# Kernel tuning notes

Measured on AMD Instinct MI355X. Metric: run time of the kernel, lower is better.

The kernel has to match this reference:

```python
import jax, jax.numpy as jnp
import numpy as np

B, T, C = 16, 1024, 768
H = 12
D = C // H  # 64 head dim


def setup_inputs() -> dict:
    key = jax.random.key(0)
    k1, k2, k3, k4, k5 = jax.random.split(key, 5)
    s = 0.02
    return {
        "x": jax.random.normal(k1, (B, T, C), dtype=jnp.float32),
        "w_attn": jax.random.normal(k2, (C, 3 * C), dtype=jnp.float32) * s,
        "b_attn": jax.random.normal(k3, (3 * C,), dtype=jnp.float32) * s,
        "w_proj": jax.random.normal(k4, (C, C), dtype=jnp.float32) * s,
        "b_proj": jax.random.normal(k5, (C,), dtype=jnp.float32) * s,
    }


def reference(x, w_attn, b_attn, w_proj, b_proj):
    Bc, Tc, Cc = x.shape
    qkv = x @ w_attn + b_attn  # [B,T,3C]
    q, k, v = jnp.split(qkv, 3, axis=-1)
    # [B,T,C] -> [B,H,T,D]
    q = q.reshape(Bc, Tc, H, D).transpose(0, 2, 1, 3)
    k = k.reshape(Bc, Tc, H, D).transpose(0, 2, 1, 3)
    v = v.reshape(Bc, Tc, H, D).transpose(0, 2, 1, 3)
    scale = 1.0 / np.sqrt(D).astype(np.float32)
    atn = jnp.einsum("bhqd,bhkd->bhqk", q, k) * scale
    causal = jnp.tril(jnp.ones((Tc, Tc), dtype=bool))
    atn = jnp.where(causal[None, None], atn, -jnp.inf)
    atn = jax.nn.softmax(atn, axis=-1)
    y = jnp.einsum("bhqk,bhkd->bhqd", atn, v)
    y = y.transpose(0, 2, 1, 3).reshape(Bc, Tc, Cc)
    return y @ w_proj + b_proj
```

## Files before the change

### kernel.cpp

```cpp
#include <hip/hip_runtime.h>
#include <hip/hip_bf16.h>

typedef __attribute__((ext_vector_type(4))) float f32x4;
typedef __attribute__((ext_vector_type(8))) short s16x8;
typedef __attribute__((ext_vector_type(4))) short s16x4;

#define AS1 __attribute__((address_space(1)))
#define AS3 __attribute__((address_space(3)))

__device__ __forceinline__ short f2bf(float f) {
    union { float f; unsigned u; } a; a.f = f;
    unsigned r = a.u + 0x7fff + ((a.u >> 16) & 1);
    return (short)(r >> 16);
}

__device__ __forceinline__ unsigned pk_bf16(float a, float b) {
    unsigned r;
    asm("v_cvt_pk_bf16_f32 %0, %1, %2" : "=v"(r) : "v"(a), "v"(b));
    return r;
}


__global__ __launch_bounds__(256) void convert_f32_bf16(const float* __restrict__ in,
                                                        short* __restrict__ out, int n4) {
    int i = blockIdx.x * 256 + threadIdx.x;
    if (i < n4) {
        f32x4 v = *(const f32x4*)(in + (long)i * 4);
        s16x4 o;
        o.x = f2bf(v.x); o.y = f2bf(v.y); o.z = f2bf(v.z); o.w = f2bf(v.w);
        *(s16x4*)(out + (long)i * 4) = o;
    }
}

__global__ __launch_bounds__(256) void transpose_w(const float* __restrict__ src,
                                                   short* __restrict__ dst, int K, int N) {
    __shared__ short t[64][65];
    int k0 = blockIdx.x * 64, n0 = blockIdx.y * 64;
    int tid = threadIdx.x;
    for (int i = tid; i < 64 * 64; i += 256) {
        int r = i >> 6, c = i & 63;
        t[r][c] = f2bf(src[(long)(k0 + r) * N + n0 + c]);
    }
    __syncthreads();
    for (int i = tid; i < 64 * 64; i += 256) {
        int r = i >> 6, c = i & 63;
        dst[(long)(n0 + r) * K + k0 + c] = t[c][r];
    }
}

__global__ __launch_bounds__(256) void transpose_vp(const short* __restrict__ vp,
                                                    short* __restrict__ vt) {
    __shared__ short t[64][72];
    int t0 = blockIdx.x * 64;
    int g = blockIdx.y;
    int tid = threadIdx.x;
#pragma unroll
    for (int i = 0; i < 2; ++i) {
        int j = tid + i * 256;
        int r = j >> 3, c = j & 7;
        s16x8 v = *(const s16x8*)(vp + ((long)g * 1024 + t0 + r) * 64 + c * 8);
#pragma unroll
        for (int e = 0; e < 8; ++e) t[c * 8 + e][r] = v[e];
    }
    __syncthreads();
#pragma unroll
    for (int i = 0; i < 2; ++i) {
        int j = tid + i * 256;
        int r = j >> 3, c = j & 7;
        *(s16x8*)(vt + ((long)g * 64 + r) * 1024 + t0 + c * 8) = *(const s16x8*)&t[r][c * 8];
    }
}


template <int MODE>
__global__ __launch_bounds__(256) void gemm_bt(const short* __restrict__ A,
                                               const short* __restrict__ BT,
                                               const float* __restrict__ bias,
                                               float* __restrict__ outF,
                                               short* __restrict__ q_,
                                               short* __restrict__ k_,
                                               short* __restrict__ v_,
                                               int M, int N, int K) {
    __shared__ short lA[128 * 32];
    __shared__ short lB[128 * 32];
    int tid = threadIdx.x;
    int lane = tid & 63, w = tid >> 6;
    int wr = w >> 1, wc = w & 1;
    int lo = lane & 15, hi = lane >> 4;
    int m0 = blockIdx.y * 128, n0 = blockIdx.x * 128;

    f32x4 acc[4][4];
#pragma unroll
    for (int i = 0; i < 4; ++i)
#pragma unroll
        for (int j = 0; j < 4; ++j) acc[i][j] = (f32x4){0.f, 0.f, 0.f, 0.f};

    const short* Abase = A + (long)m0 * K;
    const short* Bbase = BT + (long)n0 * K;

    for (int k0 = 0; k0 < K; k0 += 32) {
        __syncthreads();
#pragma unroll
        for (int i = 0; i < 2; ++i) {
            int c = (w * 2 + i) * 64 + lane;
            const short* ga = Abase + (long)(c >> 2) * K + k0 + (c & 3) * 8;
            const short* gb = Bbase + (long)(c >> 2) * K + k0 + (c & 3) * 8;
            __builtin_amdgcn_global_load_lds((const AS1 void*)ga,
                                             (AS3 void*)(lA + (w * 2 + i) * 512), 16, 0, 0);
            __builtin_amdgcn_global_load_lds((const AS1 void*)gb,
                                             (AS3 void*)(lB + (w * 2 + i) * 512), 16, 0, 0);
        }
        __syncthreads();

        s16x8 a[4], b[4];
#pragma unroll
        for (int mi = 0; mi < 4; ++mi)
            a[mi] = *(const s16x8*)(lA + (wr * 64 + mi * 16 + lo) * 32 + hi * 8);
#pragma unroll
        for (int ni = 0; ni < 4; ++ni)
            b[ni] = *(const s16x8*)(lB + (wc * 64 + ni * 16 + lo) * 32 + hi * 8);
#pragma unroll
        for (int mi = 0; mi < 4; ++mi)
#pragma unroll
            for (int ni = 0; ni < 4; ++ni)
                acc[mi][ni] = __builtin_amdgcn_mfma_f32_16x16x32_bf16(a[mi], b[ni], acc[mi][ni], 0, 0, 0);
    }

#pragma unroll
    for (int mi = 0; mi < 4; ++mi)
#pragma unroll
        for (int ni = 0; ni < 4; ++ni)
#pragma unroll
            for (int r = 0; r < 4; ++r) {
                int gm = m0 + wr * 64 + mi * 16 + hi * 4 + r;
                int gn = n0 + wc * 64 + ni * 16 + lo;
                float v = acc[mi][ni][r] + bias[gn];
                if (MODE == 1) {
                    int part = gn / 768;
                    int hh = (gn - part * 768) >> 6;
                    int dd = gn & 63;
                    long gi = (((long)(gm >> 10) * 12 + hh) * 1024 + (gm & 1023)) * 64 + dd;
                    if (part == 0) q_[gi] = f2bf(v * 0.180336880f);
                    else if (part == 1) k_[gi] = f2bf(v);
                    else v_[gi] = f2bf(v);
                } else {
                    outF[(long)gm * N + gn] = v;
                }
            }
}


__device__ __forceinline__ void attn_tile(const short* __restrict__ Kb,
                                          const short* __restrict__ Vb,
                                          int kv0, int qb0, bool diag,
                                          s16x8 bq0, s16x8 bq1,
                                          f32x4 (&ov)[4], float& mrun, float& lrun,
                                          int lo, int hi, int hi2, int sA, int sB,
                                          int sl0, int sl1) {
    f32x4 s[4];
#pragma unroll
    for (int n = 0; n < 4; ++n) {
        const short* kr = Kb + (n * 16 + lo) * 64;
        s16x8 kf0 = *(const s16x8*)(kr + sl0);
        s16x8 kf1 = *(const s16x8*)(kr + sl1);
        f32x4 t = (f32x4){0.f, 0.f, 0.f, 0.f};
        t = __builtin_amdgcn_mfma_f32_16x16x32_bf16(kf0, bq0, t, 0, 0, 0);
        t = __builtin_amdgcn_mfma_f32_16x16x32_bf16(kf1, bq1, t, 0, 0, 0);
        s[n] = t;
    }
    s16x8 av0[4], av1[4];
#pragma unroll
    for (int nd = 0; nd < 4; ++nd) {
        const short* vr = Vb + (nd * 16 + lo) * 64;
        av0[nd] = *(const s16x8*)(vr + sl0);
        av1[nd] = *(const s16x8*)(vr + sl1);
    }

    int qglob = qb0 + lo;
    if (diag) {
#pragma unroll
        for (int n = 0; n < 4; ++n)
#pragma unroll
            for (int r = 0; r < 4; ++r)
                if (kv0 + n * 16 + hi * 4 + r > qglob) s[n][r] = -3.0e38f;
    }
    float mx = s[0][0];
#pragma unroll
    for (int n = 0; n < 4; ++n)
#pragma unroll
        for (int r = 0; r < 4; ++r) mx = fmaxf(mx, s[n][r]);
    mx = fmaxf(mx, __shfl_xor(mx, 16));
    mx = fmaxf(mx, __shfl_xor(mx, 32));
    float mn = fmaxf(mrun, mx);
    float alpha = exp2f(mrun - mn);
    mrun = mn;
    float rs = 0.f;
#pragma unroll
    for (int n = 0; n < 4; ++n)
#pragma unroll
        for (int r = 0; r < 4; ++r) {
            float p = exp2f(s[n][r] - mn);
            s[n][r] = p;
            rs += p;
        }
    rs += __shfl_xor(rs, 16);
    rs += __shfl_xor(rs, 32);
    lrun = lrun * alpha + rs;
#pragma unroll
    for (int nd = 0; nd < 4; ++nd)
#pragma unroll
        for (int r = 0; r < 4; ++r) ov[nd][r] *= alpha;

    unsigned W[4][2];
#pragma unroll
    for (int n = 0; n < 4; ++n) {
        W[n][0] = pk_bf16(s[n][0], s[n][1]);
        W[n][1] = pk_bf16(s[n][2], s[n][3]);
    }
    s16x8 ap[2];
#pragma unroll
    for (int kc = 0; kc < 2; ++kc) {
        unsigned a0 = __shfl(W[kc * 2][0], sA), b0 = __shfl(W[kc * 2 + 1][0], sA);
        unsigned a1 = __shfl(W[kc * 2][1], sA), b1 = __shfl(W[kc * 2 + 1][1], sA);
        unsigned a2 = __shfl(W[kc * 2][0], sB), b2 = __shfl(W[kc * 2 + 1][0], sB);
        unsigned a3 = __shfl(W[kc * 2][1], sB), b3 = __shfl(W[kc * 2 + 1][1], sB);
        union { unsigned u[4]; s16x8 v; } cv;
        cv.u[0] = hi2 ? b0 : a0;
        cv.u[1] = hi2 ? b1 : a1;
        cv.u[2] = hi2 ? b2 : a2;
        cv.u[3] = hi2 ? b3 : a3;
        ap[kc] = cv.v;
    }
#pragma unroll
    for (int nd = 0; nd < 4; ++nd) {
        ov[nd] = __builtin_amdgcn_mfma_f32_16x16x32_bf16(av0[nd], ap[0], ov[nd], 0, 0, 0);
        ov[nd] = __builtin_amdgcn_mfma_f32_16x16x32_bf16(av1[nd], ap[1], ov[nd], 0, 0, 0);
    }
}

__device__ __forceinline__ void store_out(const f32x4 (&ov)[4], float lrun,
                                          long rowbase, int qb0, int h,
                                          int lo, int hi, short* __restrict__ y) {
    float inv = 1.0f / lrun;
    long row = (rowbase + qb0 + lo) * 768 + h * 64;
#pragma unroll
    for (int nd = 0; nd < 4; ++nd)
#pragma unroll
        for (int j2 = 0; j2 < 2; ++j2) {
            unsigned pv = pk_bf16(ov[nd][2 * j2] * inv, ov[nd][2 * j2 + 1] * inv);
            *(unsigned*)(y + row + nd * 16 + hi * 4 + 2 * j2) = pv;
        }
}

__global__ __launch_bounds__(256) void flash_attn7(const short* __restrict__ qpk,
                                                   const short* __restrict__ kpk,
                                                   const short* __restrict__ vtg,
                                                   short* __restrict__ y) {
    __shared__ short Kb[2][4096];
    __shared__ short Vb[2][4096];

    int d = blockIdx.x;
    int qp = d / 192, g = d % 192;
    int h = g % 12, b = g / 12;
    int tid = threadIdx.x, lane = tid & 63, w = tid >> 6;
    int lo = lane & 15, hi = lane >> 4, hi2 = hi >> 1;
    long rowbase = (long)b * 1024;
    const short* kb_g = kpk + (long)g * 65536;
    const short* vt_g = vtg + (long)g * 65536;
    int sA = ((hi & 1) * 2) * 16 + lo, sB = sA + 16;

    int rl = lane >> 3;
    int cs8 = (((lane & 7) ^ rl)) * 8;
    int r0 = w * 8 + rl;
    int sl0 = (hi ^ (lo & 7)) * 8;
    int sl1 = ((hi + 4) ^ (lo & 7)) * 8;

    int qbA = qp * 64 + w * 16;
    int qbB = (15 - qp) * 64 + w * 16;

    f32x4 ov[4];
    float mrun = -3.0e38f, lrun = 0.f;
#pragma unroll
    for (int nd = 0; nd < 4; ++nd) ov[nd] = (f32x4){0.f, 0.f, 0.f, 0.f};
    s16x8 bq0, bq1;
    {
        const short* qrow = qpk + ((long)g * 1024 + qbA + lo) * 64;
        bq0 = *(const s16x8*)(qrow + hi * 8);
        bq1 = *(const s16x8*)(qrow + 32 + hi * 8);
    }

#define STAGE(kv0_, buf_)                                                                    \
    do {                                                                                     \
        _Pragma("unroll")                                                                    \
        for (int i_ = 0; i_ < 2; ++i_) {                                                     \
            int r_ = i_ * 32 + r0;                                                           \
            __builtin_amdgcn_global_load_lds(                                                \
                (const AS1 void*)(kb_g + (long)((kv0_) + r_) * 64 + cs8),                    \
                (AS3 void*)(Kb[buf_] + (i_ * 32 + w * 8) * 64), 16, 0, 0);                   \
            __builtin_amdgcn_global_load_lds(                                                \
                (const AS1 void*)(vt_g + (long)r_ * 1024 + (kv0_) + cs8),                    \
                (AS3 void*)(Vb[buf_] + (i_ * 32 + w * 8) * 64), 16, 0, 0);                   \
        }                                                                                    \
    } while (0)

    STAGE(0, 0);
    __syncthreads();

    int cur = 0;
    for (int u = 0; u < 17; ++u) {
        int nu = u + 1;
        if (nu < 17) {
            int nkv0 = (nu <= qp) ? nu * 64 : (nu - qp - 1) * 64;
            STAGE(nkv0, cur ^ 1);
        }
        bool phaseA = (u <= qp);
        int kv0 = phaseA ? u * 64 : (u - qp - 1) * 64;
        int qb0 = phaseA ? qbA : qbB;
        bool diag = phaseA ? (u == qp) : (u == 16);
        attn_tile(Kb[cur], Vb[cur], kv0, qb0, diag, bq0, bq1, ov, mrun, lrun,
                  lo, hi, hi2, sA, sB, sl0, sl1);
        if (phaseA && u == qp) {
            store_out(ov, lrun, rowbase, qbA, h, lo, hi, y);
            const short* qrow = qpk + ((long)g * 1024 + qbB + lo) * 64;
            bq0 = *(const s16x8*)(qrow + hi * 8);
            bq1 = *(const s16x8*)(qrow + 32 + hi * 8);
#pragma unroll
            for (int nd = 0; nd < 4; ++nd) ov[nd] = (f32x4){0.f, 0.f, 0.f, 0.f};
            mrun = -3.0e38f; lrun = 0.f;
        }
        __syncthreads();
        cur ^= 1;
    }
    store_out(ov, lrun, rowbase, qbB, h, lo, hi, y);
#undef STAGE
}


extern "C" void kernel_launch(void* const* d_in, const int* in_sizes, int n_in,
                              void* d_out, int out_size, void* d_ws, size_t ws_size,
                              hipStream_t stream) {
    const float* x      = (const float*)d_in[0];
    const float* w_attn = (const float*)d_in[1];
    const float* b_attn = (const float*)d_in[2];
    const float* w_proj = (const float*)d_in[3];
    const float* b_proj = (const float*)d_in[4];

    char* ws = (char*)d_ws;
    short* x_bf = (short*)ws;
    short* qpk  = (short*)(ws + 25165824);
    short* kpk  = (short*)(ws + 50331648);
    short* vpk  = (short*)(ws + 75497472);
    short* yb   = (short*)(ws + 100663296);
    short* waT  = (short*)(ws + 125829120);
    short* wpT  = (short*)(ws + 129368064);
    short* vt   = x_bf;

    convert_f32_bf16<<<dim3(12288), dim3(256), 0, stream>>>(x, x_bf, 3145728);
    transpose_w<<<dim3(12, 36), dim3(256), 0, stream>>>(w_attn, waT, 768, 2304);
    transpose_w<<<dim3(12, 12), dim3(256), 0, stream>>>(w_proj, wpT, 768, 768);
    gemm_bt<1><<<dim3(18, 128), dim3(256), 0, stream>>>(x_bf, waT, b_attn,
                                                        (float*)nullptr, qpk, kpk, vpk,
                                                        16384, 2304, 768);
    transpose_vp<<<dim3(16, 192), dim3(256), 0, stream>>>(vpk, vt);
    flash_attn7<<<dim3(1536), dim3(256), 0, stream>>>(qpk, kpk, vt, yb);
    gemm_bt<0><<<dim3(6, 128), dim3(256), 0, stream>>>(yb, wpT, b_proj,
                                                       (float*)d_out, (short*)nullptr,
                                                       (short*)nullptr, (short*)nullptr,
                                                       16384, 768, 768);
}
```

Before: 238.1 us.

## Rewrite GEMM as 256x256 tile, 8-wave double-buffered pipelined kernel with swizzled LDS

Replaces the 128x128, 4-wave GEMM, which synchronised twice per K step, with a 256x256 tile computed by 512 threads. Global-to-LDS loads are double-buffered and issued ahead of use, with vmcnt waits and raw barriers instead of __syncthreads. The LDS layout is XOR-swizzled to avoid bank conflicts, and s_setprio is raised around the MFMA blocks. This targets load latency and barrier stalls in the QKV and projection GEMMs. The cost is far fewer blocks (576 and 192), which risks poor occupancy across the CUs, especially for the projection GEMM.

```diff
diff --git a/kernel.cpp b/kernel.cpp
--- a/kernel.cpp
+++ b/kernel.cpp
@@ -73,67 +73,108 @@
 
 
 template <int MODE>
-__global__ __launch_bounds__(256) void gemm_bt(const short* __restrict__ A,
-                                               const short* __restrict__ BT,
-                                               const float* __restrict__ bias,
-                                               float* __restrict__ outF,
-                                               short* __restrict__ q_,
-                                               short* __restrict__ k_,
-                                               short* __restrict__ v_,
-                                               int M, int N, int K) {
-    __shared__ short lA[128 * 32];
-    __shared__ short lB[128 * 32];
+__global__ __launch_bounds__(512, 2) void gemm_bt(const short* __restrict__ A,
+                                                  const short* __restrict__ BT,
+                                                  const float* __restrict__ bias,
+                                                  float* __restrict__ outF,
+                                                  short* __restrict__ q_,
+                                                  short* __restrict__ k_,
+                                                  short* __restrict__ v_,
+                                                  int M, int N, int K) {
+    __shared__ short As[2 * 2 * 64 * 64];
+    __shared__ short Bs[2 * 2 * 64 * 64];
+
     int tid = threadIdx.x;
     int lane = tid & 63, w = tid >> 6;
-    int wr = w >> 1, wc = w & 1;
+    int wm = w >> 2, wn = w & 3;
     int lo = lane & 15, hi = lane >> 4;
-    int m0 = blockIdx.y * 128, n0 = blockIdx.x * 128;
-
-    f32x4 acc[4][4];
-#pragma unroll
-    for (int i = 0; i < 4; ++i)
+    int m0 = blockIdx.y * 256, n0 = blockIdx.x * 256;
+    int T = K >> 5;
+
+    int srlo = lo >> 1;
+    int aoff = srlo * 64 + ((((lo & 1) << 2) + hi) ^ srlo) * 8;
+
+    int srl = w * 8 + (lane >> 3);
+    int cc = (lane & 7) ^ (lane >> 3);
+    int growoff = cc >> 2;
+    int gcoloff = (cc & 3) * 8;
+
+    const short* Ag = A + (long)m0 * K;
+    const short* Bg = BT + (long)n0 * K;
+
+    f32x4 acc[8][4];
+#pragma unroll
+    for (int i = 0; i < 8; ++i)
 #pragma unroll
         for (int j = 0; j < 4; ++j) acc[i][j] = (f32x4){0.f, 0.f, 0.f, 0.f};
 
-    const short* Abase = A + (long)m0 * K;
-    const short* Bbase = BT + (long)n0 * K;
-
-    for (int k0 = 0; k0 < K; k0 += 32) {
-        __syncthreads();
-#pragma unroll
-        for (int i = 0; i < 2; ++i) {
-            int c = (w * 2 + i) * 64 + lane;
-            const short* ga = Abase + (long)(c >> 2) * K + k0 + (c & 3) * 8;
-            const short* gb = Bbase + (long)(c >> 2) * K + k0 + (c & 3) * 8;
-            __builtin_amdgcn_global_load_lds((const AS1 void*)ga,
-                                             (AS3 void*)(lA + (w * 2 + i) * 512), 16, 0, 0);
-            __builtin_amdgcn_global_load_lds((const AS1 void*)gb,
-                                             (AS3 void*)(lB + (w * 2 + i) * 512), 16, 0, 0);
+    auto stage = [&](int tt, const short* G, short* Ls, int eta) {
+        const short* src = G + (long)(eta * 128 + srl * 2 + growoff) * K + tt * 32 + gcoloff;
+        short* dst = Ls + (((tt & 1) * 2 + eta) * 64 + w * 8) * 64;
+        __builtin_amdgcn_global_load_lds((const AS1 void*)src, (AS3 void*)dst, 16, 0, 0);
+    };
+
+    stage(0, Ag, As, 0); stage(0, Ag, As, 1);
+    stage(0, Bg, Bs, 0); stage(0, Bg, Bs, 1);
+    stage(1, Bg, Bs, 0); stage(1, Bg, Bs, 1);
+    stage(1, Ag, As, 0);
+    asm volatile("s_waitcnt vmcnt(3)" ::: "memory");
+    __builtin_amdgcn_s_barrier();
+
+    for (int t = 0; t < T; ++t) {
+        int buf = t & 1;
+        s16x8 bfr[4], afr[4];
+#pragma unroll
+        for (int ni = 0; ni < 4; ++ni)
+            bfr[ni] = *(const s16x8*)(Bs + ((buf * 2 + (wn >> 1)) * 64 + (wn & 1) * 32 + ni * 8) * 64 + aoff);
+#pragma unroll
+        for (int mi = 0; mi < 4; ++mi)
+            afr[mi] = *(const s16x8*)(As + ((buf * 2 + 0) * 64 + wm * 32 + mi * 8) * 64 + aoff);
+        if (t + 1 < T) stage(t + 1, Ag, As, 1);
+        __builtin_amdgcn_s_barrier();
+        asm volatile("s_waitcnt lgkmcnt(0)" ::: "memory");
+        __builtin_amdgcn_sched_barrier(0);
+        __builtin_amdgcn_s_setprio(1);
+#pragma unroll
+        for (int mi = 0; mi < 4; ++mi)
+#pragma unroll
+            for (int ni = 0; ni < 4; ++ni)
+                acc[mi][ni] = __builtin_amdgcn_mfma_f32_16x16x32_bf16(afr[mi], bfr[ni], acc[mi][ni], 0, 0, 0);
+        __builtin_amdgcn_s_setprio(0);
+        __builtin_amdgcn_s_barrier();
+
+#pragma unroll
+        for (int mi = 0; mi < 4; ++mi)
+            afr[mi] = *(const s16x8*)(As + ((buf * 2 + 1) * 64 + wm * 32 + mi * 8) * 64 + aoff);
+        if (t + 2 < T) {
+            stage(t + 2, Bg, Bs, 0);
+            stage(t + 2, Bg, Bs, 1);
+            stage(t + 2, Ag, As, 0);
+            asm volatile("s_waitcnt vmcnt(3)" ::: "memory");
+        } else if (t + 1 < T) {
+            asm volatile("s_waitcnt vmcnt(0)" ::: "memory");
         }
-        __syncthreads();
-
-        s16x8 a[4], b[4];
+        __builtin_amdgcn_s_barrier();
+        asm volatile("s_waitcnt lgkmcnt(0)" ::: "memory");
+        __builtin_amdgcn_sched_barrier(0);
+        __builtin_amdgcn_s_setprio(1);
 #pragma unroll
         for (int mi = 0; mi < 4; ++mi)
-            a[mi] = *(const s16x8*)(lA + (wr * 64 + mi * 16 + lo) * 32 + hi * 8);
+#pragma unroll
+            for (int ni = 0; ni < 4; ++ni)
+                acc[mi + 4][ni] = __builtin_amdgcn_mfma_f32_16x16x32_bf16(afr[mi], bfr[ni], acc[mi + 4][ni], 0, 0, 0);
+        __builtin_amdgcn_s_setprio(0);
+        __builtin_amdgcn_s_barrier();
+    }
+
+#pragma unroll
+    for (int mi = 0; mi < 8; ++mi)
 #pragma unroll
         for (int ni = 0; ni < 4; ++ni)
-            b[ni] = *(const s16x8*)(lB + (wc * 64 + ni * 16 + lo) * 32 + hi * 8);
-#pragma unroll
-        for (int mi = 0; mi < 4; ++mi)
-#pragma unroll
-            for (int ni = 0; ni < 4; ++ni)
-                acc[mi][ni] = __builtin_amdgcn_mfma_f32_16x16x32_bf16(a[mi], b[ni], acc[mi][ni], 0, 0, 0);
-    }
-
-#pragma unroll
-    for (int mi = 0; mi < 4; ++mi)
-#pragma unroll
-        for (int ni = 0; ni < 4; ++ni)
 #pragma unroll
             for (int r = 0; r < 4; ++r) {
-                int gm = m0 + wr * 64 + mi * 16 + hi * 4 + r;
-                int gn = n0 + wc * 64 + ni * 16 + lo;
+                int gm = m0 + (mi >> 2) * 128 + wm * 64 + (mi & 3) * 16 + hi * 4 + r;
+                int gn = n0 + wn * 64 + ni * 16 + lo;
                 float v = acc[mi][ni][r] + bias[gn];
                 if (MODE == 1) {
                     int part = gn / 768;
@@ -358,13 +399,13 @@
     convert_f32_bf16<<<dim3(12288), dim3(256), 0, stream>>>(x, x_bf, 3145728);
     transpose_w<<<dim3(12, 36), dim3(256), 0, stream>>>(w_attn, waT, 768, 2304);
     transpose_w<<<dim3(12, 12), dim3(256), 0, stream>>>(w_proj, wpT, 768, 768);
-    gemm_bt<1><<<dim3(18, 128), dim3(256), 0, stream>>>(x_bf, waT, b_attn,
-                                                        (float*)nullptr, qpk, kpk, vpk,
-                                                        16384, 2304, 768);
+    gemm_bt<1><<<dim3(9, 64), dim3(512), 0, stream>>>(x_bf, waT, b_attn,
+                                                      (float*)nullptr, qpk, kpk, vpk,
+                                                      16384, 2304, 768);
     transpose_vp<<<dim3(16, 192), dim3(256), 0, stream>>>(vpk, vt);
     flash_attn7<<<dim3(1536), dim3(256), 0, stream>>>(qpk, kpk, vt, yb);
-    gemm_bt<0><<<dim3(6, 128), dim3(256), 0, stream>>>(yb, wpT, b_proj,
-                                                       (float*)d_out, (short*)nullptr,
-                                                       (short*)nullptr, (short*)nullptr,
-                                                       16384, 768, 768);
-}
+    gemm_bt<0><<<dim3(3, 64), dim3(512), 0, stream>>>(yb, wpT, b_proj,
+                                                      (float*)d_out, (short*)nullptr,
+                                                      (short*)nullptr, (short*)nullptr,
+                                                      16384, 768, 768);
+}
```

Result: slower. 251.4 us (+5.6%).

## Restructure GEMM with K=64 steps, XOR-swizzled LDS, XCD block swizzle, hoisted epilogue

Applied to the files above, without the earlier changes.

The GEMM kernel now stages 64 elements of K per iteration as two 32-wide sub-tiles, halving the number of barrier pairs. The LDS layout packs two logical rows per 64-element row and XORs the column chunk to avoid bank conflicts on fragment reads. Blocks use a 1D grid remapped so consecutive blocks land on the same XCD (bid&7 interleave), which should improve L2 reuse. The epilogue hoists bias loads and the per-element q/k/v partition math out of the inner loop. The cost is more complex indexing, and the swizzle assumes the grid size is divisible by 8.

```diff
diff --git a/kernel.cpp b/kernel.cpp
--- a/kernel.cpp
+++ b/kernel.cpp
@@ -81,13 +81,18 @@
                                                short* __restrict__ k_,
                                                short* __restrict__ v_,
                                                int M, int N, int K) {
-    __shared__ short lA[128 * 32];
-    __shared__ short lB[128 * 32];
+    __shared__ short lA[2 * 64 * 64];
+    __shared__ short lB[2 * 64 * 64];
     int tid = threadIdx.x;
     int lane = tid & 63, w = tid >> 6;
     int wr = w >> 1, wc = w & 1;
     int lo = lane & 15, hi = lane >> 4;
-    int m0 = blockIdx.y * 128, n0 = blockIdx.x * 128;
+
+    int bid = blockIdx.x;
+    int swz = (bid & 7) * ((int)gridDim.x >> 3) + (bid >> 3);
+    int NX = N >> 7;
+    int bx = swz % NX, by = swz / NX;
+    int m0 = by * 128, n0 = bx * 128;
 
     f32x4 acc[4][4];
 #pragma unroll
@@ -98,55 +103,85 @@
     const short* Abase = A + (long)m0 * K;
     const short* Bbase = BT + (long)n0 * K;
 
-    for (int k0 = 0; k0 < K; k0 += 32) {
+    int lr = lane >> 3;
+    int cc = (lane & 7) ^ lr;
+    int growoff = cc >> 2;
+    int gcol = (cc & 3) * 8;
+
+    int srlo = lo >> 1;
+    int rpar = (lo & 1) << 2;
+
+    for (int k0 = 0; k0 < K; k0 += 64) {
         __syncthreads();
 #pragma unroll
-        for (int i = 0; i < 2; ++i) {
-            int c = (w * 2 + i) * 64 + lane;
-            const short* ga = Abase + (long)(c >> 2) * K + k0 + (c & 3) * 8;
-            const short* gb = Bbase + (long)(c >> 2) * K + k0 + (c & 3) * 8;
-            __builtin_amdgcn_global_load_lds((const AS1 void*)ga,
-                                             (AS3 void*)(lA + (w * 2 + i) * 512), 16, 0, 0);
-            __builtin_amdgcn_global_load_lds((const AS1 void*)gb,
-                                             (AS3 void*)(lB + (w * 2 + i) * 512), 16, 0, 0);
+        for (int kk = 0; kk < 2; ++kk)
+#pragma unroll
+            for (int j = 0; j < 2; ++j) {
+                int sr = w * 16 + j * 8 + lr;
+                long grow = (long)(sr * 2 + growoff);
+                const short* ga = Abase + grow * K + k0 + kk * 32 + gcol;
+                const short* gb = Bbase + grow * K + k0 + kk * 32 + gcol;
+                short* da = lA + kk * 4096 + (w * 16 + j * 8) * 64;
+                short* db = lB + kk * 4096 + (w * 16 + j * 8) * 64;
+                __builtin_amdgcn_global_load_lds((const AS1 void*)ga, (AS3 void*)da, 16, 0, 0);
+                __builtin_amdgcn_global_load_lds((const AS1 void*)gb, (AS3 void*)db, 16, 0, 0);
+            }
+        __syncthreads();
+
+#pragma unroll
+        for (int kk = 0; kk < 2; ++kk) {
+            s16x8 a[4], b[4];
+#pragma unroll
+            for (int mi = 0; mi < 4; ++mi)
+                a[mi] = *(const s16x8*)(lA + kk * 4096 + (wr * 32 + mi * 8 + srlo) * 64 +
+                                        ((rpar + hi) ^ srlo) * 8);
+#pragma unroll
+            for (int ni = 0; ni < 4; ++ni)
+                b[ni] = *(const s16x8*)(lB + kk * 4096 + (wc * 32 + ni * 8 + srlo) * 64 +
+                                        ((rpar + hi) ^ srlo) * 8);
+#pragma unroll
+            for (int mi = 0; mi < 4; ++mi)
+#pragma unroll
+                for (int ni = 0; ni < 4; ++ni)
+                    acc[mi][ni] = __builtin_amdgcn_mfma_f32_16x16x32_bf16(a[mi], b[ni], acc[mi][ni], 0, 0, 0);
         }
-        __syncthreads();
-
-        s16x8 a[4], b[4];
+    }
+
+    float bs[4];
+#pragma unroll
+    for (int ni = 0; ni < 4; ++ni) bs[ni] = bias[n0 + wc * 64 + ni * 16 + lo];
+
+    if (MODE == 1) {
+        int blk = (n0 + wc * 64) >> 6;
+        int part = (blk >= 24) ? 2 : (blk >= 12 ? 1 : 0);
+        int hh = blk - part * 12;
+        short* dst = (part == 0) ? q_ : (part == 1) ? k_ : v_;
+        float scl = (part == 0) ? 0.180336880f : 1.0f;
+        int bidx = m0 >> 10;
+        int trow0 = (m0 & 1023) + wr * 64;
+        long gb_ = ((long)(bidx * 12 + hh)) << 16;
 #pragma unroll
         for (int mi = 0; mi < 4; ++mi)
-            a[mi] = *(const s16x8*)(lA + (wr * 64 + mi * 16 + lo) * 32 + hi * 8);
-#pragma unroll
-        for (int ni = 0; ni < 4; ++ni)
-            b[ni] = *(const s16x8*)(lB + (wc * 64 + ni * 16 + lo) * 32 + hi * 8);
+#pragma unroll
+            for (int ni = 0; ni < 4; ++ni)
+#pragma unroll
+                for (int r = 0; r < 4; ++r) {
+                    int trow = trow0 + mi * 16 + hi * 4 + r;
+                    float v = (acc[mi][ni][r] + bs[ni]) * scl;
+                    dst[gb_ + (long)trow * 64 + ni * 16 + lo] = f2bf(v);
+                }
+    } else {
 #pragma unroll
         for (int mi = 0; mi < 4; ++mi)
 #pragma unroll
             for (int ni = 0; ni < 4; ++ni)
-                acc[mi][ni] = __builtin_amdgcn_mfma_f32_16x16x32_bf16(a[mi], b[ni], acc[mi][ni], 0, 0, 0);
-    }
-
-#pragma unroll
-    for (int mi = 0; mi < 4; ++mi)
-#pragma unroll
-        for (int ni = 0; ni < 4; ++ni)
-#pragma unroll
-            for (int r = 0; r < 4; ++r) {
-                int gm = m0 + wr * 64 + mi * 16 + hi * 4 + r;
-                int gn = n0 + wc * 64 + ni * 16 + lo;
-                float v = acc[mi][ni][r] + bias[gn];
-                if (MODE == 1) {
-                    int part = gn / 768;
-                    int hh = (gn - part * 768) >> 6;
-                    int dd = gn & 63;
-                    long gi = (((long)(gm >> 10) * 12 + hh) * 1024 + (gm & 1023)) * 64 + dd;
-                    if (part == 0) q_[gi] = f2bf(v * 0.180336880f);
-                    else if (part == 1) k_[gi] = f2bf(v);
-                    else v_[gi] = f2bf(v);
-                } else {
-                    outF[(long)gm * N + gn] = v;
+#pragma unroll
+                for (int r = 0; r < 4; ++r) {
+                    int gm = m0 + wr * 64 + mi * 16 + hi * 4 + r;
+                    int gn = n0 + wc * 64 + ni * 16 + lo;
+                    outF[(long)gm * N + gn] = acc[mi][ni][r] + bs[ni];
                 }
-            }
+    }
 }
 
 
@@ -358,13 +393,13 @@
     convert_f32_bf16<<<dim3(12288), dim3(256), 0, stream>>>(x, x_bf, 3145728);
     transpose_w<<<dim3(12, 36), dim3(256), 0, stream>>>(w_attn, waT, 768, 2304);
     transpose_w<<<dim3(12, 12), dim3(256), 0, stream>>>(w_proj, wpT, 768, 768);
-    gemm_bt<1><<<dim3(18, 128), dim3(256), 0, stream>>>(x_bf, waT, b_attn,
-                                                        (float*)nullptr, qpk, kpk, vpk,
-                                                        16384, 2304, 768);
+    gemm_bt<1><<<dim3(2304), dim3(256), 0, stream>>>(x_bf, waT, b_attn,
+                                                     (float*)nullptr, qpk, kpk, vpk,
+                                                     16384, 2304, 768);
     transpose_vp<<<dim3(16, 192), dim3(256), 0, stream>>>(vpk, vt);
     flash_attn7<<<dim3(1536), dim3(256), 0, stream>>>(qpk, kpk, vt, yb);
-    gemm_bt<0><<<dim3(6, 128), dim3(256), 0, stream>>>(yb, wpT, b_proj,
-                                                       (float*)d_out, (short*)nullptr,
-                                                       (short*)nullptr, (short*)nullptr,
-                                                       16384, 768, 768);
-}
+    gemm_bt<0><<<dim3(768), dim3(256), 0, stream>>>(yb, wpT, b_proj,
+                                                    (float*)d_out, (short*)nullptr,
+                                                    (short*)nullptr, (short*)nullptr,
+                                                    16384, 768, 768);
+}
```

New measurement: 214.8 us. 1.11x faster.
